# Kernel optimization log

Measured on AMD Instinct MI355X. Metric: run time of the kernel, lower is better.

## Reference

```python
import jax, jax.numpy as jnp
import numpy as np

NHEADS = 16  # init kwarg


def setup_inputs() -> dict:
    key = jax.random.key(0)
    ks = jax.random.split(key, 3)
    S, B, E = 2048, 4, 1024
    x = jax.random.normal(ks[0], (S, B, E), dtype=jnp.float32)
    Wqkv = jax.random.normal(ks[1], (E, 3 * E), dtype=jnp.float32) * 0.02
    bqkv = jnp.zeros((3 * E,), dtype=jnp.float32)
    Wout = jax.random.normal(ks[2], (E, E), dtype=jnp.float32) * 0.02
    bout = jnp.zeros((E,), dtype=jnp.float32)
    return {"x": x, "Wqkv": Wqkv, "bqkv": bqkv, "Wout": Wout, "bout": bout}


def reference(x, Wqkv, bqkv, Wout, bout):
    S, B, E = x.shape
    H = NHEADS
    d = E // H
    scale = jnp.sqrt(jnp.asarray(E / H, dtype=x.dtype))  # sqrt(d_head)
    qkv = x @ Wqkv + bqkv                      # (S, B, 3E)
    q, k, v = jnp.split(qkv, 3, axis=-1)       # each (S, B, E)
    # (S, B, E) -> (S, B*H, d) -> (B*H, S, d), matching torch reshape+permute
    q = q.reshape(S, B * H, d).transpose(1, 0, 2)
    k = k.reshape(S, B * H, d).transpose(1, 0, 2)
    v = v.reshape(S, B * H, d).transpose(1, 0, 2)
    scores = jnp.einsum('hsd,htd->hst', q, k) / scale  # (B*H, S, S)
    attn = jax.nn.softmax(scores, axis=-1)
    o = jnp.einsum('hst,htd->hsd', attn, v)    # (B*H, S, d)
    o = o.transpose(1, 0, 2).reshape(S, B, E)  # back to (S, B, E)
    return o @ Wout + bout
```

## Files before the change

kernel.cpp:

```cpp
#include <hip/hip_runtime.h>

typedef short s16x8 __attribute__((ext_vector_type(8)));
typedef float f32x4 __attribute__((ext_vector_type(4)));
typedef unsigned int u32x2 __attribute__((ext_vector_type(2)));

__device__ inline float bf2f(unsigned short u) {
    union { float f; unsigned int i; } x; x.i = ((unsigned int)u) << 16; return x.f;
}
__device__ inline unsigned short f2bf(float f) {
    union { float f; unsigned int i; } x; x.f = f;
    unsigned int r = x.i + 0x7fff + ((x.i >> 16) & 1);
    return (unsigned short)(r >> 16);
}
__device__ inline unsigned int pack_bf16(float a, float b) {
    unsigned int ia = __float_as_uint(a) + 0x8000u;
    unsigned int ib = __float_as_uint(b) + 0x8000u;
    return (ia >> 16) | (ib & 0xffff0000u);
}

__device__ inline void gload_lds16(const unsigned short* g, unsigned short* l) {
    __builtin_amdgcn_global_load_lds(
        (const __attribute__((address_space(1))) unsigned int*)g,
        (__attribute__((address_space(3))) unsigned int*)l, 16, 0, 0);
}

__global__ void detect_dtype(const unsigned short* __restrict__ x16, int* flag) {
    __shared__ int s[256];
    int tid = threadIdx.x;
    int cnt = 0;
    for (int i = tid; i < 4096; i += 256) {
        unsigned short u = x16[2 * i];
        int e = (u >> 7) & 0xFF;
        if (e >= 117 && e <= 129) cnt++;
    }
    s[tid] = cnt;
    __syncthreads();
    for (int off = 128; off; off >>= 1) {
        if (tid < off) s[tid] += s[tid + off];
        __syncthreads();
    }
    if (tid == 0) *flag = (s[0] < 2048) ? 1 : 0;
}

__global__ void convert_x(const void* __restrict__ in, unsigned short* __restrict__ out,
                          const int* __restrict__ flag, int n) {
    int mode = *flag;
    int i0 = (blockIdx.x * 256 + threadIdx.x) * 8;
    if (i0 >= n) return;
    if (mode) {
        const float* f = (const float*)in;
#pragma unroll
        for (int j = 0; j < 8; ++j) out[i0 + j] = f2bf(f[i0 + j]);
    } else {
        *(s16x8*)(out + i0) = *(const s16x8*)((const unsigned short*)in + i0);
    }
}

__global__ void cvt_bias(const void* __restrict__ in, float* __restrict__ out,
                         const int* __restrict__ flag, int n) {
    int i = blockIdx.x * 256 + threadIdx.x;
    if (i >= n) return;
    out[i] = (*flag) ? ((const float*)in)[i] : bf2f(((const unsigned short*)in)[i]);
}

__global__ void transpose_cvt(const void* __restrict__ in, unsigned short* __restrict__ out,
                              const int* __restrict__ flag, int R, int C) {
    __shared__ unsigned short t[64][72];
    int mode = *flag;
    int r0 = blockIdx.y * 64, c0 = blockIdx.x * 64;
    for (int i = threadIdx.x; i < 64 * 64; i += 256) {
        int r = i >> 6, c = i & 63;
        size_t idx = (size_t)(r0 + r) * C + (c0 + c);
        t[r][c] = mode ? f2bf(((const float*)in)[idx]) : ((const unsigned short*)in)[idx];
    }
    __syncthreads();
    for (int i = threadIdx.x; i < 64 * 64; i += 256) {
        int c = i >> 6, r = i & 63;
        out[(size_t)(c0 + c) * R + (r0 + r)] = t[r][c];
    }
}

__global__ __launch_bounds__(256) void transpose_v(
    const unsigned short* __restrict__ qkv, unsigned short* __restrict__ Vt) {
    __shared__ unsigned short t[64][72];
    int bh = blockIdx.y; int b = bh >> 4, h = bh & 15;
    int k0 = blockIdx.x * 64;
    int tid = threadIdx.x;
    int kr = tid >> 2, db = (tid & 3) * 16;
    const unsigned short* src = qkv + ((size_t)(k0 + kr) * 4 + b) * 3072 + 2048 + h * 64 + db;
    *(s16x8*)&t[kr][db] = *(const s16x8*)src;
    *(s16x8*)&t[kr][db + 8] = *(const s16x8*)(src + 8);
    __syncthreads();
    int d = tid >> 2, kb = (tid & 3) * 16;
    unsigned short* dst = Vt + (size_t)bh * 131072 + (size_t)d * 2048 + k0 + kb;
    s16x8 a, c;
#pragma unroll
    for (int j = 0; j < 8; ++j) a[j] = t[kb + j][d];
#pragma unroll
    for (int j = 0; j < 8; ++j) c[j] = t[kb + 8 + j][d];
    *(s16x8*)dst = a;
    *(s16x8*)(dst + 8) = c;
}

__global__ __launch_bounds__(512) void gemm_pipe_kernel(
    const unsigned short* __restrict__ A, const unsigned short* __restrict__ BT,
    const float* __restrict__ bias, void* __restrict__ Cout,
    int M, int N, int K, int qcols, float qscale, const int* __restrict__ outf32flag) {
    __shared__ unsigned short As[3][256 * 64];
    __shared__ unsigned short Bs[3][128 * 64];
    int tid = threadIdx.x;
    int lane = tid & 63, w = tid >> 6;
    int wr = w >> 1, wc = w & 1;
    int g = lane >> 4, qh = lane & 15;
    int m0 = blockIdx.y * 256, n0 = blockIdx.x * 128;
    int vxor = (lane & 7) ^ (lane >> 3);
    int axor = qh & 7;

    f32x4 z = {0.f, 0.f, 0.f, 0.f};
    f32x4 acc[4][4];
#pragma unroll
    for (int m = 0; m < 4; ++m)
#pragma unroll
        for (int n = 0; n < 4; ++n) acc[m][n] = z;

    const unsigned short* Asrc = A + (size_t)(m0 + w * 8 + (lane >> 3)) * K + vxor * 8;
    const unsigned short* Bsrc = BT + (size_t)(n0 + w * 8 + (lane >> 3)) * K + vxor * 8;

#define STAGE_A(buf, t, j) gload_lds16(Asrc + (size_t)(j) * 64 * K + (size_t)(t) * 64, \
                                       &As[buf][0] + (j) * 4096 + w * 512)
#define STAGE_B(buf, t, j) gload_lds16(Bsrc + (size_t)(j) * 64 * K + (size_t)(t) * 64, \
                                       &Bs[buf][0] + (j) * 4096 + w * 512)

    int NT = K >> 6;
    STAGE_A(0, 0, 0); STAGE_A(0, 0, 1); STAGE_A(0, 0, 2); STAGE_A(0, 0, 3);
    STAGE_B(0, 0, 0); STAGE_B(0, 0, 1);
    STAGE_A(1, 1, 0); STAGE_A(1, 1, 1); STAGE_A(1, 1, 2); STAGE_A(1, 1, 3);
    STAGE_B(1, 1, 0); STAGE_B(1, 1, 1);
    asm volatile("s_waitcnt vmcnt(6)" ::: "memory");
    __builtin_amdgcn_s_barrier();

    int cur = 0;
    for (int t = 0; t < NT; ++t) {
        int nx = cur + 2; if (nx >= 3) nx -= 3;
        bool pf = (t + 2) < NT;
        const unsigned short* Ab = &As[cur][0];
        const unsigned short* Bb = &Bs[cur][0];

        s16x8 bf[4][2];
#pragma unroll
        for (int n = 0; n < 4; ++n)
#pragma unroll
            for (int kk = 0; kk < 2; ++kk)
                bf[n][kk] = *(const s16x8*)(Bb + (size_t)(wc * 64 + n * 16 + qh) * 64 +
                                            (((kk * 4 + g) ^ axor) * 8));

        if (pf) { STAGE_A(nx, t + 2, 0); STAGE_A(nx, t + 2, 1); STAGE_B(nx, t + 2, 0); }
        {
            s16x8 af[2][2];
#pragma unroll
            for (int i = 0; i < 2; ++i)
#pragma unroll
                for (int kk = 0; kk < 2; ++kk)
                    af[i][kk] = *(const s16x8*)(Ab + (size_t)(wr * 64 + i * 16 + qh) * 64 +
                                                (((kk * 4 + g) ^ axor) * 8));
            __builtin_amdgcn_s_setprio(1);
#pragma unroll
            for (int kk = 0; kk < 2; ++kk)
#pragma unroll
                for (int i = 0; i < 2; ++i)
#pragma unroll
                    for (int n = 0; n < 4; ++n)
                        acc[i][n] = __builtin_amdgcn_mfma_f32_16x16x32_bf16(af[i][kk], bf[n][kk], acc[i][n], 0, 0, 0);
            __builtin_amdgcn_s_setprio(0);
        }
        __builtin_amdgcn_s_barrier();

        if (pf) { STAGE_A(nx, t + 2, 2); STAGE_A(nx, t + 2, 3); STAGE_B(nx, t + 2, 1); }
        {
            s16x8 af[2][2];
#pragma unroll
            for (int i = 0; i < 2; ++i)
#pragma unroll
                for (int kk = 0; kk < 2; ++kk)
                    af[i][kk] = *(const s16x8*)(Ab + (size_t)(wr * 64 + (i + 2) * 16 + qh) * 64 +
                                                (((kk * 4 + g) ^ axor) * 8));
            __builtin_amdgcn_s_setprio(1);
#pragma unroll
            for (int kk = 0; kk < 2; ++kk)
#pragma unroll
                for (int i = 0; i < 2; ++i)
#pragma unroll
                    for (int n = 0; n < 4; ++n)
                        acc[i + 2][n] = __builtin_amdgcn_mfma_f32_16x16x32_bf16(af[i][kk], bf[n][kk], acc[i + 2][n], 0, 0, 0);
            __builtin_amdgcn_s_setprio(0);
        }
        if (t + 1 < NT) {
            if (pf) asm volatile("s_waitcnt vmcnt(6)" ::: "memory");
            else    asm volatile("s_waitcnt vmcnt(0)" ::: "memory");
            __builtin_amdgcn_s_barrier();
        }
        cur = cur + 1; if (cur >= 3) cur -= 3;
    }
#undef STAGE_A
#undef STAGE_B

    bool f32out = (outf32flag != nullptr) && (*outf32flag != 0);
    int crow0 = m0 + wr * 64;
    int ccol0 = n0 + wc * 64;
#pragma unroll
    for (int n = 0; n < 4; ++n) {
        int col = ccol0 + n * 16 + qh;
        float bv = bias[col];
        float qs = (col < qcols) ? qscale : 1.0f;
#pragma unroll
        for (int m = 0; m < 4; ++m) {
            int rbase = crow0 + m * 16 + g * 4;
#pragma unroll
            for (int qq = 0; qq < 4; ++qq) {
                float v = (acc[m][n][qq] + bv) * qs;
                if (f32out)
                    ((float*)Cout)[(size_t)(rbase + qq) * N + col] = v;
                else
                    ((unsigned short*)Cout)[(size_t)(rbase + qq) * N + col] = f2bf(v);
            }
        }
    }
}

__global__ __launch_bounds__(256) void attn_kernel(
    const unsigned short* __restrict__ qkv, const unsigned short* __restrict__ Vt,
    unsigned short* __restrict__ O) {
    int bh = blockIdx.y;
    int b = bh >> 4, h = bh & 15;
    int q0 = blockIdx.x * 128;
    int tid = threadIdx.x, lane = tid & 63, w = tid >> 6;
    int g = lane >> 4, qh = lane & 15;

    __shared__ unsigned short Ks[8 * 64 * 8];
    __shared__ unsigned short Vs[64 * 64];
    __shared__ unsigned short Pb[4][2][16 * 64];

    s16x8 qf[2][2];
#pragma unroll
    for (int qs = 0; qs < 2; ++qs) {
        int qrow = q0 + w * 32 + qs * 16 + qh;
        const unsigned short* qp = qkv + ((size_t)qrow * 4 + b) * 3072 + h * 64 + g * 8;
        qf[qs][0] = *(const s16x8*)qp;
        qf[qs][1] = *(const s16x8*)(qp + 32);
    }

    f32x4 z = {0.f, 0.f, 0.f, 0.f};
    f32x4 oacc[2][4];
#pragma unroll
    for (int qs = 0; qs < 2; ++qs)
#pragma unroll
        for (int dt = 0; dt < 4; ++dt) oacc[qs][dt] = z;
    float lrun[2] = {0.f, 0.f};

    int vxor = (lane & 7) ^ (lane >> 3);

    for (int k0 = 0; k0 < 2048; k0 += 64) {
        __syncthreads();
        {
            const unsigned short* ksrc = qkv + ((size_t)(k0 + lane) * 4 + b) * 3072 + 1024 + h * 64;
            gload_lds16(ksrc + w * 8, Ks + (size_t)w * 512);
            gload_lds16(ksrc + (w + 4) * 8, Ks + (size_t)(w + 4) * 512);
        }
#pragma unroll
        for (int c = 0; c < 2; ++c) {
            int d = (c * 4 + w) * 8 + (lane >> 3);
            const unsigned short* vsrc = Vt + (size_t)bh * 131072 + (size_t)d * 2048 + k0 + vxor * 8;
            gload_lds16(vsrc, Vs + (size_t)(c * 4 + w) * 512);
        }
        __syncthreads();

        f32x4 sc[2][4];
#pragma unroll
        for (int qs = 0; qs < 2; ++qs)
#pragma unroll
            for (int ct = 0; ct < 4; ++ct) sc[qs][ct] = z;
#pragma unroll
        for (int kk = 0; kk < 2; ++kk)
#pragma unroll
            for (int ct = 0; ct < 4; ++ct) {
                s16x8 kf = *(const s16x8*)(Ks + ((size_t)(kk * 4 + g) * 64 + ct * 16 + qh) * 8);
                sc[0][ct] = __builtin_amdgcn_mfma_f32_16x16x32_bf16(kf, qf[0][kk], sc[0][ct], 0, 0, 0);
                sc[1][ct] = __builtin_amdgcn_mfma_f32_16x16x32_bf16(kf, qf[1][kk], sc[1][ct], 0, 0, 0);
            }

#pragma unroll
        for (int qs = 0; qs < 2; ++qs) {
            float rsum = 0.f;
            unsigned short* pwq = &Pb[w][qs][0];
#pragma unroll
            for (int ct = 0; ct < 4; ++ct) {
                float p0 = __builtin_amdgcn_exp2f(sc[qs][ct][0]);
                float p1 = __builtin_amdgcn_exp2f(sc[qs][ct][1]);
                float p2 = __builtin_amdgcn_exp2f(sc[qs][ct][2]);
                float p3 = __builtin_amdgcn_exp2f(sc[qs][ct][3]);
                rsum += (p0 + p1) + (p2 + p3);
                u32x2 pv;
                pv[0] = pack_bf16(p0, p1);
                pv[1] = pack_bf16(p2, p3);
                int blk = ct * 2 + (g >> 1);
                int e = qh * 64 + ((blk ^ (qh & 7)) * 8) + (g & 1) * 4;
                *(u32x2*)(pwq + e) = pv;
            }
            rsum += __shfl_xor(rsum, 16);
            rsum += __shfl_xor(rsum, 32);
            lrun[qs] += rsum;
        }

        asm volatile("s_waitcnt lgkmcnt(0)" ::: "memory");
        __builtin_amdgcn_sched_barrier(0);

#pragma unroll
        for (int kk2 = 0; kk2 < 2; ++kk2) {
            int blkr = ((kk2 * 4 + g) ^ (qh & 7)) * 8;
            s16x8 pb0 = *(const s16x8*)(&Pb[w][0][0] + qh * 64 + blkr);
            s16x8 pb1 = *(const s16x8*)(&Pb[w][1][0] + qh * 64 + blkr);
#pragma unroll
            for (int dt = 0; dt < 4; ++dt) {
                s16x8 vtf = *(const s16x8*)(Vs + (size_t)(dt * 16 + qh) * 64 + blkr);
                oacc[0][dt] = __builtin_amdgcn_mfma_f32_16x16x32_bf16(vtf, pb0, oacc[0][dt], 0, 0, 0);
                oacc[1][dt] = __builtin_amdgcn_mfma_f32_16x16x32_bf16(vtf, pb1, oacc[1][dt], 0, 0, 0);
            }
        }
    }

#pragma unroll
    for (int qs = 0; qs < 2; ++qs) {
        float rl = 1.f / lrun[qs];
        int s = q0 + w * 32 + qs * 16 + qh;
        unsigned short* orow = O + ((size_t)s * 4 + b) * 1024 + h * 64;
#pragma unroll
        for (int dt = 0; dt < 4; ++dt) {
            u32x2 pv;
            pv[0] = pack_bf16(oacc[qs][dt][0] * rl, oacc[qs][dt][1] * rl);
            pv[1] = pack_bf16(oacc[qs][dt][2] * rl, oacc[qs][dt][3] * rl);
            *(u32x2*)(orow + dt * 16 + g * 4) = pv;
        }
    }
}

extern "C" void kernel_launch(void* const* d_in, const int* in_sizes, int n_in,
                              void* d_out, int out_size, void* d_ws, size_t ws_size,
                              hipStream_t stream) {
    const void* x    = d_in[0];
    const void* Wqkv = d_in[1];
    const void* bqkv = d_in[2];
    const void* Wout = d_in[3];
    const void* bout = d_in[4];

    char* ws = (char*)d_ws;
    unsigned short* qkv   = (unsigned short*)(ws);
    unsigned short* Obuf  = (unsigned short*)(ws + 50331648);
    unsigned short* WqkvT = (unsigned short*)(ws + 67108864);
    unsigned short* WoutT = (unsigned short*)(ws + 73400320);
    unsigned short* xb    = (unsigned short*)(ws + 75497472);
    unsigned short* Vtg   = xb;
    float*          bq_f  = (float*)(ws + 92274688);
    float*          bo_f  = (float*)(ws + 92286976);
    int*            flag  = (int*)(ws + 92291072);

    detect_dtype<<<1, 256, 0, stream>>>((const unsigned short*)x, flag);
    convert_x<<<4096, 256, 0, stream>>>(x, xb, flag, 8388608);
    cvt_bias<<<12, 256, 0, stream>>>(bqkv, bq_f, flag, 3072);
    cvt_bias<<<4, 256, 0, stream>>>(bout, bo_f, flag, 1024);
    transpose_cvt<<<dim3(48, 16), 256, 0, stream>>>(Wqkv, WqkvT, flag, 1024, 3072);
    transpose_cvt<<<dim3(16, 16), 256, 0, stream>>>(Wout, WoutT, flag, 1024, 1024);

    gemm_pipe_kernel<<<dim3(24, 32), 512, 0, stream>>>(xb, WqkvT, bq_f, qkv,
                                                       8192, 3072, 1024, 1024, 0.18033688f, nullptr);
    transpose_v<<<dim3(32, 64), 256, 0, stream>>>(qkv, Vtg);
    attn_kernel<<<dim3(16, 64), 256, 0, stream>>>(qkv, Vtg, Obuf);
    gemm_pipe_kernel<<<dim3(8, 32), 512, 0, stream>>>(Obuf, WoutT, bo_f, d_out,
                                                      8192, 1024, 1024, 0, 1.0f, flag);
}
```

Baseline: 286.4 us.

## Switch attention to 32x32x16 MFMA with in-register P via permlane32_swap

Rewrites the attention inner loop to use 32x32x16 bf16 MFMA tiles instead of 16x16x32, with each wave handling 32 query rows as one tile. The softmax probabilities are repacked in registers with permlane32_swap to form the B operand of the PV MFMA, which removes the shared-memory P buffer round trip and its waitcnt barrier. It also drops one of the cross-lane shuffle reductions. The cost is larger accumulator fragments and different LDS access patterns for K and V reads, which may create bank conflicts or raise register pressure.

```diff
diff --git a/kernel.cpp b/kernel.cpp
--- a/kernel.cpp
+++ b/kernel.cpp
@@ -2,6 +2,7 @@
 
 typedef short s16x8 __attribute__((ext_vector_type(8)));
 typedef float f32x4 __attribute__((ext_vector_type(4)));
+typedef float f32x16 __attribute__((ext_vector_type(16)));
 typedef unsigned int u32x2 __attribute__((ext_vector_type(2)));
 
 __device__ inline float bf2f(unsigned short u) {
@@ -234,28 +235,21 @@
     int b = bh >> 4, h = bh & 15;
     int q0 = blockIdx.x * 128;
     int tid = threadIdx.x, lane = tid & 63, w = tid >> 6;
-    int g = lane >> 4, qh = lane & 15;
+    int l31 = lane & 31, l5 = lane >> 5;
 
     __shared__ unsigned short Ks[8 * 64 * 8];
     __shared__ unsigned short Vs[64 * 64];
-    __shared__ unsigned short Pb[4][2][16 * 64];
-
-    s16x8 qf[2][2];
-#pragma unroll
-    for (int qs = 0; qs < 2; ++qs) {
-        int qrow = q0 + w * 32 + qs * 16 + qh;
-        const unsigned short* qp = qkv + ((size_t)qrow * 4 + b) * 3072 + h * 64 + g * 8;
-        qf[qs][0] = *(const s16x8*)qp;
-        qf[qs][1] = *(const s16x8*)(qp + 32);
-    }
-
-    f32x4 z = {0.f, 0.f, 0.f, 0.f};
-    f32x4 oacc[2][4];
-#pragma unroll
-    for (int qs = 0; qs < 2; ++qs)
-#pragma unroll
-        for (int dt = 0; dt < 4; ++dt) oacc[qs][dt] = z;
-    float lrun[2] = {0.f, 0.f};
+
+    int qrow = q0 + w * 32 + l31;
+    const unsigned short* qp = qkv + ((size_t)qrow * 4 + b) * 3072 + h * 64 + l5 * 8;
+    s16x8 qf[4];
+#pragma unroll
+    for (int st = 0; st < 4; ++st) qf[st] = *(const s16x8*)(qp + st * 16);
+
+    f32x16 z16 = {0.f,0.f,0.f,0.f,0.f,0.f,0.f,0.f,0.f,0.f,0.f,0.f,0.f,0.f,0.f,0.f};
+    f32x16 oacc[2];
+    oacc[0] = z16; oacc[1] = z16;
+    float lrun = 0.f;
 
     int vxor = (lane & 7) ^ (lane >> 3);
 
@@ -274,71 +268,64 @@
         }
         __syncthreads();
 
-        f32x4 sc[2][4];
-#pragma unroll
-        for (int qs = 0; qs < 2; ++qs)
-#pragma unroll
-            for (int ct = 0; ct < 4; ++ct) sc[qs][ct] = z;
-#pragma unroll
-        for (int kk = 0; kk < 2; ++kk)
-#pragma unroll
-            for (int ct = 0; ct < 4; ++ct) {
-                s16x8 kf = *(const s16x8*)(Ks + ((size_t)(kk * 4 + g) * 64 + ct * 16 + qh) * 8);
-                sc[0][ct] = __builtin_amdgcn_mfma_f32_16x16x32_bf16(kf, qf[0][kk], sc[0][ct], 0, 0, 0);
-                sc[1][ct] = __builtin_amdgcn_mfma_f32_16x16x32_bf16(kf, qf[1][kk], sc[1][ct], 0, 0, 0);
+        f32x16 sc[2];
+        sc[0] = z16; sc[1] = z16;
+#pragma unroll
+        for (int st = 0; st < 4; ++st) {
+            int gd = st * 2 + l5;
+#pragma unroll
+            for (int kt = 0; kt < 2; ++kt) {
+                s16x8 kf = *(const s16x8*)(Ks + ((size_t)(gd * 64 + kt * 32 + l31)) * 8);
+                sc[kt] = __builtin_amdgcn_mfma_f32_32x32x16_bf16(kf, qf[st], sc[kt], 0, 0, 0);
             }
-
-#pragma unroll
-        for (int qs = 0; qs < 2; ++qs) {
-            float rsum = 0.f;
-            unsigned short* pwq = &Pb[w][qs][0];
-#pragma unroll
-            for (int ct = 0; ct < 4; ++ct) {
-                float p0 = __builtin_amdgcn_exp2f(sc[qs][ct][0]);
-                float p1 = __builtin_amdgcn_exp2f(sc[qs][ct][1]);
-                float p2 = __builtin_amdgcn_exp2f(sc[qs][ct][2]);
-                float p3 = __builtin_amdgcn_exp2f(sc[qs][ct][3]);
-                rsum += (p0 + p1) + (p2 + p3);
-                u32x2 pv;
-                pv[0] = pack_bf16(p0, p1);
-                pv[1] = pack_bf16(p2, p3);
-                int blk = ct * 2 + (g >> 1);
-                int e = qh * 64 + ((blk ^ (qh & 7)) * 8) + (g & 1) * 4;
-                *(u32x2*)(pwq + e) = pv;
+        }
+
+        float rsum = 0.f;
+#pragma unroll
+        for (int kt = 0; kt < 2; ++kt) {
+            float p[16];
+#pragma unroll
+            for (int r = 0; r < 16; ++r) {
+                p[r] = __builtin_amdgcn_exp2f(sc[kt][r]);
+                rsum += p[r];
             }
-            rsum += __shfl_xor(rsum, 16);
-            rsum += __shfl_xor(rsum, 32);
-            lrun[qs] += rsum;
-        }
-
-        asm volatile("s_waitcnt lgkmcnt(0)" ::: "memory");
-        __builtin_amdgcn_sched_barrier(0);
-
-#pragma unroll
-        for (int kk2 = 0; kk2 < 2; ++kk2) {
-            int blkr = ((kk2 * 4 + g) ^ (qh & 7)) * 8;
-            s16x8 pb0 = *(const s16x8*)(&Pb[w][0][0] + qh * 64 + blkr);
-            s16x8 pb1 = *(const s16x8*)(&Pb[w][1][0] + qh * 64 + blkr);
-#pragma unroll
-            for (int dt = 0; dt < 4; ++dt) {
-                s16x8 vtf = *(const s16x8*)(Vs + (size_t)(dt * 16 + qh) * 64 + blkr);
-                oacc[0][dt] = __builtin_amdgcn_mfma_f32_16x16x32_bf16(vtf, pb0, oacc[0][dt], 0, 0, 0);
-                oacc[1][dt] = __builtin_amdgcn_mfma_f32_16x16x32_bf16(vtf, pb1, oacc[1][dt], 0, 0, 0);
+#pragma unroll
+            for (int ks1 = 0; ks1 < 2; ++ks1) {
+                unsigned int A0 = pack_bf16(p[8 * ks1 + 0], p[8 * ks1 + 1]);
+                unsigned int A1 = pack_bf16(p[8 * ks1 + 2], p[8 * ks1 + 3]);
+                unsigned int B0 = pack_bf16(p[8 * ks1 + 4], p[8 * ks1 + 5]);
+                unsigned int B1 = pack_bf16(p[8 * ks1 + 6], p[8 * ks1 + 7]);
+                u32x2 r0 = __builtin_amdgcn_permlane32_swap(A0, B0, false, false);
+                u32x2 r1 = __builtin_amdgcn_permlane32_swap(A1, B1, false, false);
+                union { unsigned int u[4]; s16x8 v; } uu;
+                uu.u[0] = r0[0];
+                uu.u[1] = r1[0];
+                uu.u[2] = r0[1];
+                uu.u[3] = r1[1];
+                int ks = kt * 2 + ks1;
+#pragma unroll
+                for (int dt = 0; dt < 2; ++dt) {
+                    int d = dt * 32 + l31;
+                    int kb = (ks * 2 + l5) ^ (d & 7);
+                    s16x8 vf = *(const s16x8*)(Vs + (size_t)d * 64 + kb * 8);
+                    oacc[dt] = __builtin_amdgcn_mfma_f32_32x32x16_bf16(vf, uu.v, oacc[dt], 0, 0, 0);
+                }
             }
         }
-    }
-
-#pragma unroll
-    for (int qs = 0; qs < 2; ++qs) {
-        float rl = 1.f / lrun[qs];
-        int s = q0 + w * 32 + qs * 16 + qh;
-        unsigned short* orow = O + ((size_t)s * 4 + b) * 1024 + h * 64;
-#pragma unroll
-        for (int dt = 0; dt < 4; ++dt) {
+        rsum += __shfl_xor(rsum, 32);
+        lrun += rsum;
+    }
+
+    float rl = 1.f / lrun;
+    unsigned short* orow = O + ((size_t)qrow * 4 + b) * 1024 + h * 64 + l5 * 4;
+#pragma unroll
+    for (int dt = 0; dt < 2; ++dt) {
+#pragma unroll
+        for (int g2 = 0; g2 < 4; ++g2) {
             u32x2 pv;
-            pv[0] = pack_bf16(oacc[qs][dt][0] * rl, oacc[qs][dt][1] * rl);
-            pv[1] = pack_bf16(oacc[qs][dt][2] * rl, oacc[qs][dt][3] * rl);
-            *(u32x2*)(orow + dt * 16 + g * 4) = pv;
+            pv[0] = pack_bf16(oacc[dt][4 * g2 + 0] * rl, oacc[dt][4 * g2 + 1] * rl);
+            pv[1] = pack_bf16(oacc[dt][4 * g2 + 2] * rl, oacc[dt][4 * g2 + 3] * rl);
+            *(u32x2*)(orow + dt * 32 + g2 * 8) = pv;
         }
     }
 }
```

Result: no change. 282.8 us (-1.3%).
